# Performance work log

Measured on AMD Instinct MI355X. Metric: run time of the kernel, lower is better.

Reference implementation:

```python
import jax, jax.numpy as jnp
from jax import lax
import numpy as np

B, S, D, COMP = 4, 1024, 512, 4


def setup_inputs() -> dict:
    key = jax.random.key(0)
    x = jax.random.normal(key, (B * S, D), dtype=jnp.float32)
    return {"x": x, "comp_rate": COMP, "seqlen": S}


def _merge_step(x, t, seq):
    # x: [seq, D], compacted so the k = seq - t valid tokens occupy rows 0..k-1.
    xn = jnp.roll(x, -1, axis=0)  # x[i+1] (wrap value never selected among valid pairs)
    # dist only feeds argmax (non-differentiable), mirror torch exactly; stop_gradient
    # keeps the vjp from saving residuals for this dead-for-gradients path.
    xg = lax.stop_gradient(x)
    dist = jnp.sum(xg * jnp.roll(xg, -1, axis=0), axis=-1)  # scalar_product metric
    j = jnp.arange(x.shape[0])
    dist = jnp.where(j < seq - 1 - t, dist, -jnp.inf)  # k-1 valid adjacent pairs
    mid = jnp.argmax(dist)
    jm = j[:, None]
    # rows < mid keep, row mid becomes (x[mid]+x[mid+1])/2, rows > mid shift left by 1
    return jnp.where(jm < mid, x, jnp.where(jm == mid, (x + xn) * 0.5, xn))


def _merge_sample(x, steps, seq):
    def body(carry, t):
        return _merge_step(carry, t, seq), None
    x, _ = lax.scan(body, x, jnp.arange(steps))
    return x


def reference(x, comp_rate, seqlen):
    d = x.shape[-1]
    b = x.shape[0] // seqlen
    n_comp = seqlen // comp_rate
    steps = seqlen - n_comp
    xb = x.reshape(b, seqlen, d)
    merged = jax.vmap(lambda xs: _merge_sample(xs, steps, seqlen))(xb)
    # torch smart_merge concatenates per-sample results along dim 0
    return merged[:, :n_comp].reshape(b * n_comp, d)
```

## Files before the change

### kernel.cpp

```cpp
#include <hip/hip_runtime.h>
#include <math.h>

#define S 1024
#define D 512
#define NCOMP (S / 4)
#define STEPS (S - NCOMP)
#define NEG_INF (-__builtin_inff())

__device__ __forceinline__ int   f2i(float x) { return __builtin_bit_cast(int, x); }
__device__ __forceinline__ float i2f(int x)   { return __builtin_bit_cast(float, x); }
__device__ __forceinline__ int   rfl(int x)   { return __builtin_amdgcn_readfirstlane(x); }

__device__ __forceinline__ unsigned fkey(float f) {
    unsigned u = __builtin_bit_cast(unsigned, f);
    return (u & 0x80000000u) ? ~u : (u | 0x80000000u);
}
__device__ __forceinline__ float unfkey(unsigned k) {
    unsigned u = (k & 0x80000000u) ? (k & 0x7fffffffu) : ~k;
    return __builtin_bit_cast(float, u);
}

__device__ __forceinline__ float wave_sum63(float x) {
    x += i2f(__builtin_amdgcn_update_dpp(0, f2i(x), 0x111, 0xF, 0xF, true));
    x += i2f(__builtin_amdgcn_update_dpp(0, f2i(x), 0x112, 0xF, 0xF, true));
    x += i2f(__builtin_amdgcn_update_dpp(0, f2i(x), 0x114, 0xF, 0xF, true));
    x += i2f(__builtin_amdgcn_update_dpp(0, f2i(x), 0x118, 0xF, 0xF, true));
    x += i2f(__builtin_amdgcn_update_dpp(0, f2i(x), 0x142, 0xA, 0xF, true));
    x += i2f(__builtin_amdgcn_update_dpp(0, f2i(x), 0x143, 0xC, 0xF, true));
    return x;
}

#define AMAX_STEP(ctrl, rm) do {                                                        \
    unsigned ok_ = (unsigned)__builtin_amdgcn_update_dpp((int)key, (int)key, (ctrl), (rm), 0xF, false); \
    int      oi_ = __builtin_amdgcn_update_dpp(bi, bi, (ctrl), (rm), 0xF, false);        \
    bool tk_ = (ok_ > key) || ((ok_ == key) && (oi_ < bi));                              \
    key = tk_ ? ok_ : key; bi = tk_ ? oi_ : bi;                                          \
} while (0)

struct Row { float4 a, b; };

__device__ __forceinline__ Row row_load(const float* vals, int slot, int lane) {
    const float4* p = (const float4*)(vals + (size_t)slot * D);
    Row r; r.a = p[lane * 2]; r.b = p[lane * 2 + 1]; return r;
}
__device__ __forceinline__ void row_store(float* vals, int slot, int lane, Row r) {
    float4* p = (float4*)(vals + (size_t)slot * D);
    p[lane * 2] = r.a; p[lane * 2 + 1] = r.b;
}
__device__ __forceinline__ Row row_avg(Row x, Row y) {
    Row r;
    r.a.x = (x.a.x + y.a.x) * 0.5f; r.a.y = (x.a.y + y.a.y) * 0.5f;
    r.a.z = (x.a.z + y.a.z) * 0.5f; r.a.w = (x.a.w + y.a.w) * 0.5f;
    r.b.x = (x.b.x + y.b.x) * 0.5f; r.b.y = (x.b.y + y.b.y) * 0.5f;
    r.b.z = (x.b.z + y.b.z) * 0.5f; r.b.w = (x.b.w + y.b.w) * 0.5f;
    return r;
}
__device__ __forceinline__ float dot8_partial(Row x, Row y) {
    float acc = x.a.x * y.a.x;
    acc += x.a.y * y.a.y; acc += x.a.z * y.a.z; acc += x.a.w * y.a.w;
    acc += x.b.x * y.b.x; acc += x.b.y * y.b.y; acc += x.b.z * y.b.z; acc += x.b.w * y.b.w;
    return acc;
}
__device__ __forceinline__ int lsr(int s) { return ((unsigned)s < (unsigned)S) ? s : 0; }
__device__ __forceinline__ int lsl(int s) { return ((unsigned)s <= (unsigned)S) ? s : 0; }

__device__ __forceinline__ void lds_argmax(const float* dist, int lane, float& v1, int& i1) {
    float av[16];
#pragma unroll
    for (int k = 0; k < 16; ++k) av[k] = dist[lane + 64 * k];
    float v8[8]; int k8[8];
#pragma unroll
    for (int k = 0; k < 8; ++k) { bool tk = av[k+8] > av[k]; v8[k] = tk ? av[k+8] : av[k]; k8[k] = tk ? (k+8) : k; }
    float v4[4]; int k4[4];
#pragma unroll
    for (int k = 0; k < 4; ++k) { bool tk = v8[k+4] > v8[k]; v4[k] = tk ? v8[k+4] : v8[k]; k4[k] = tk ? k8[k+4] : k8[k]; }
    float v2[2]; int k2[2];
#pragma unroll
    for (int k = 0; k < 2; ++k) { bool tk = v4[k+2] > v4[k]; v2[k] = tk ? v4[k+2] : v4[k]; k2[k] = tk ? k4[k+2] : k4[k]; }
    bool tk1 = v2[1] > v2[0];
    float lv = tk1 ? v2[1] : v2[0];
    int   lk = tk1 ? k2[1] : k2[0];
    unsigned key = fkey(lv);
    int bi = lane | (lk << 6);
    AMAX_STEP(0x111, 0xF); AMAX_STEP(0x112, 0xF);
    AMAX_STEP(0x114, 0xF); AMAX_STEP(0x118, 0xF);
    AMAX_STEP(0x142, 0xA); AMAX_STEP(0x143, 0xC);
    i1 = __builtin_amdgcn_readlane(bi, 63);
    v1 = unfkey((unsigned)__builtin_amdgcn_readlane((int)key, 63));
}

__global__ __launch_bounds__(256) void init_kernel(const float* __restrict__ x,
                                                   float* __restrict__ vals,
                                                   float* __restrict__ out) {
    const int blk = blockIdx.x, b = blk >> 4, g = blk & 15;
    const int tid = threadIdx.x, lane = tid & 63, w = tid >> 6;
    const float* xb = x + (size_t)b * S * D;
    if (blk == 0 && tid == 0) *(int*)(out + 2048) = 0;
    if (vals != x) {
        float* vb = vals + (size_t)b * S * D;
        const float4* s4 = (const float4*)xb;
        float4* d4 = (float4*)vb;
        const int base = g * (S * D / 4 / 16);
        for (int i = tid; i < S * D / 4 / 16; i += 256) d4[base + i] = s4[base + i];
    }
    float* sd = out + (size_t)b * NCOMP * D;
#pragma unroll 1
    for (int j = 0; j < 16; ++j) {
        int pr = g * 64 + w * 16 + j;
        if (pr < S - 1) {
            Row A = row_load(xb, pr, lane);
            Row B = row_load(xb, pr + 1, lane);
            float t = wave_sum63(dot8_partial(A, B));
            if (lane == 63) sd[pr] = t;
        }
    }
    if (g == 0 && tid == 0) sd[S - 1] = NEG_INF;
}

__global__ __launch_bounds__(256, 1) void merge_kernel(float* __restrict__ vals,
                                                       float* __restrict__ out,
                                                       int nb) {
    const int blk = blockIdx.x, tid = threadIdx.x;
    int* flag = (int*)(out + 2048);

    if (blk >= nb) {
        float a0 = (float)tid * 0.5f + 1.0f, a1 = a0 + 0.25f, a2 = a0 + 0.5f, a3 = a0 + 0.75f;
        for (;;) {
#pragma unroll
            for (int i = 0; i < 16; ++i) {
                a0 = __builtin_fmaf(a0, 1.0000001f, 1.1920929e-7f);
                a1 = __builtin_fmaf(a1, 0.9999999f, 1.1920929e-7f);
                a2 = __builtin_fmaf(a2, 1.0000002f, 1.1920929e-7f);
                a3 = __builtin_fmaf(a3, 0.9999998f, 1.1920929e-7f);
            }
            if (__hip_atomic_load(flag, __ATOMIC_RELAXED, __HIP_MEMORY_SCOPE_AGENT) >= nb)
                break;
        }
        if (a0 + a1 + a2 + a3 == 1234.5678f) out[2049] = a0;
        return;
    }

    const int b = blk, lane = tid & 63, wave = tid >> 6;
    float* vb = vals + (size_t)b * S * D;
    float* aux = out + (size_t)b * NCOMP * D;
    const float* sd = aux;
    int* outIdx = (int*)(aux + S);

    if (wave != 0) {
        float acc = 0.0f;
        for (int s = wave - 1; s < S; s += 3) {
            Row rr = row_load(vb, s, lane);
            acc += rr.a.x + rr.b.w;
        }
        if (acc == 1234.5678f) out[2050] = acc;
        return;
    }

    __shared__ int4 links[S + 1];
    __shared__ float dist[S];

    for (int s = lane; s <= S; s += 64)
        links[s] = (s >= S) ? make_int4(S, S, S, 0)
                            : make_int4(s - 1, s + 1, (s + 2 <= S) ? (s + 2) : S, 0);
#pragma unroll
    for (int k = 0; k < 16; ++k) dist[lane + 64 * k] = sd[lane + 64 * k];

    float v1; int i1;
    lds_argmax(dist, lane, v1, i1);
    int m = i1;
    int4 L0 = links[m];
    int p = rfl(L0.x);
    int r = rfl(L0.y);
    int q = rfl(L0.z);
    bool hasp = (p >= 0), hasq = (q < S);
    int pp = hasp ? rfl(links[lsl(p)].x) : -1;
    int nq = hasq ? rfl(links[lsl(q)].y) : S;
    Row Rp  = row_load(vb, lsr(p),  lane);
    Row Rm  = row_load(vb, m,       lane);
    Row Rr  = row_load(vb, r,       lane);
    Row Rq  = row_load(vb, lsr(q),  lane);
    Row Rpp = row_load(vb, lsr(pp), lane);
    Row Rnq = row_load(vb, lsr(nq), lane);

#pragma unroll 1
    for (int t = 0; t < STEPS; ++t) {
        if (lane == 0) {
            links[m].y = q; links[m].z = nq;
            if (hasp) links[p].z = q;
            if (hasq) links[q].x = m;
            dist[m] = NEG_INF; dist[r] = NEG_INF;
            if (hasp) dist[p] = NEG_INF;
        }
        Row vm = row_avg(Rm, Rr);
        row_store(vb, m, lane, vm);
        if (t + 1 >= STEPS) break;

        float sp_ = wave_sum63(dot8_partial(Rp, vm));
        float sq_ = wave_sum63(dot8_partial(vm, Rq));
        float ndp = hasp ? i2f(__builtin_amdgcn_readlane(f2i(sp_), 63)) : NEG_INF;
        float ndm = hasq ? i2f(__builtin_amdgcn_readlane(f2i(sq_), 63)) : NEG_INF;

        lds_argmax(dist, lane, v1, i1);

        float best = v1; int bi = i1;
        if (hasp && (ndp > best || (ndp == best && p < bi))) { best = ndp; bi = p; }
        if (hasq && (ndm > best || (ndm == best && m < bi))) { best = ndm; bi = m; }
        const int m2 = bi;

        if (lane == 0) {
            if (hasp) dist[p] = ndp;
            if (hasq) dist[m] = ndm;
        }

        int4 Li = links[lsl(i1)];
        int p2 = rfl(Li.x);
        int r2 = rfl(Li.y);
        int q2 = rfl(Li.z);
        int4 Lp2 = links[lsl(p2)];
        int4 Lq2 = links[lsl(q2)];
        int pp2 = (p2 >= 0) ? rfl(Lp2.x) : -1;
        int nq2 = (q2 < S)  ? rfl(Lq2.y) : S;
        Row Sp  = (p2 == m)  ? vm : row_load(vb, lsr(p2),  lane);
        Row Si  = row_load(vb, lsr(i1), lane);
        Row Sr  = row_load(vb, lsr(r2), lane);
        Row Sq  = (q2 == m)  ? vm : row_load(vb, lsr(q2),  lane);
        Row Spp = (pp2 == m) ? vm : row_load(vb, lsr(pp2), lane);
        Row Snq = (nq2 == m) ? vm : row_load(vb, lsr(nq2), lane);

        if (m2 == m) {
            int nnq = S;
            if (nq < S) nnq = rfl(links[nq].y);
            Row Rnq2 = (nnq < S) ? row_load(vb, lsr(nnq), lane) : Rnq;
            Rm = vm; Rr = Rq; Rq = Rnq; Rnq = Rnq2;
            r = q; q = nq; nq = nnq;
            hasq = (q < S);
        } else if (m2 == p) {
            int npp = -1;
            if (pp >= 0) npp = rfl(links[pp].x);
            Row Rpp2 = (npp >= 0) ? row_load(vb, lsr(npp), lane) : Rpp;
            Rr = vm; Rm = Rp; Rp = Rpp; Rpp = Rpp2;
            r = m; m = p; p = pp; pp = npp;
            hasp = (p >= 0);
        } else {
            m = i1; p = p2; r = r2; q = q2; pp = pp2; nq = nq2;
            Rm = Si; Rr = Sr; Rp = Sp; Rq = Sq; Rpp = Spp; Rnq = Snq;
            hasp = (p >= 0); hasq = (q < S);
        }
    }

    if (lane == 0) {
        int s = 0;
        for (int i = 0; i < NCOMP; i += 2) {
            outIdx[i] = s;
            int4 Ls = links[s];
            if (i + 1 < NCOMP) outIdx[i + 1] = Ls.y;
            s = Ls.z;
        }
        __hip_atomic_fetch_add(flag, 1, __ATOMIC_RELAXED, __HIP_MEMORY_SCOPE_AGENT);
    }
}

__global__ __launch_bounds__(256) void gather_kernel(const float* __restrict__ vals,
                                                     float* __restrict__ out) {
    const int b = blockIdx.x, part = blockIdx.y;
    const float* vb = vals + (size_t)b * S * D;
    float* ob = out + (size_t)b * NCOMP * D;
    __shared__ int oi[NCOMP / 8];
    const int row0 = part * (NCOMP / 8);
    if (threadIdx.x < NCOMP / 8)
        oi[threadIdx.x] = ((const int*)(ob + S))[row0 + threadIdx.x];
    __syncthreads();
    const float4* v4 = (const float4*)vb;
    float4* o4 = (float4*)ob;
    const int per = (NCOMP / 8) * (D / 4);
    for (int idx = threadIdx.x; idx < per; idx += 256) {
        int row = idx >> 7, c = idx & 127;
        o4[(size_t)(row0 + row) * (D / 4) + c] = v4[(size_t)oi[row] * (D / 4) + c];
    }
}

extern "C" void kernel_launch(void* const* d_in, const int* in_sizes, int n_in,
                              void* d_out, int out_size, void* d_ws, size_t ws_size,
                              hipStream_t stream) {
    const float* x = (const float*)d_in[0];
    float* out = (float*)d_out;
    const int b = in_sizes[0] / (S * D);
    const size_t need = (size_t)in_sizes[0] * sizeof(float);
    float* vals = (ws_size >= need) ? (float*)d_ws : (float*)x;
    init_kernel<<<dim3(16 * b), dim3(256), 0, stream>>>(x, vals, out);
    merge_kernel<<<dim3(256), dim3(256), 0, stream>>>(vals, out, b);
    gather_kernel<<<dim3(b, 8), dim3(256), 0, stream>>>(vals, out);
}
```

Baseline: 1.031 ms.

## Hoist argmax and speculative row loads ahead of merge compute in serial loop

Stores a second-predecessor link in the .w field so the pp and nnq neighbors can be looked up with fewer dependent LDS reads. Moves the LDS argmax and all candidate row loads to the start of each step, before the averaged row is computed and stored, so their latency overlaps the dot products. Rows that may be stale because the previous step's global store has not yet landed are patched from a register copy (mprev/Rprev). This issues more loads per step and adds bookkeeping that must handle aliasing correctly.

```diff
diff --git a/kernel.cpp b/kernel.cpp
--- a/kernel.cpp
+++ b/kernel.cpp
@@ -161,9 +161,11 @@
 
     for (int s = lane; s <= S; s += 64)
         links[s] = (s >= S) ? make_int4(S, S, S, 0)
-                            : make_int4(s - 1, s + 1, (s + 2 <= S) ? (s + 2) : S, 0);
+                            : make_int4(s - 1, s + 1, (s + 2 <= S) ? (s + 2) : S, s - 2);
 #pragma unroll
     for (int k = 0; k < 16; ++k) dist[lane + 64 * k] = sd[lane + 64 * k];
+
+    const int* li32 = (const int*)links;
 
     float v1; int i1;
     lds_argmax(dist, lane, v1, i1);
@@ -181,16 +183,39 @@
     Row Rq  = row_load(vb, lsr(q),  lane);
     Row Rpp = row_load(vb, lsr(pp), lane);
     Row Rnq = row_load(vb, lsr(nq), lane);
+    int mprev = -1;
+    Row Rprev = Rm;
 
 #pragma unroll 1
     for (int t = 0; t < STEPS; ++t) {
         if (lane == 0) {
             links[m].y = q; links[m].z = nq;
             if (hasp) links[p].z = q;
-            if (hasq) links[q].x = m;
+            if (hasq) { links[q].x = m; links[q].w = p; links[lsl(nq)].w = m; }
             dist[m] = NEG_INF; dist[r] = NEG_INF;
             if (hasp) dist[p] = NEG_INF;
         }
+
+        int vnnq = li32[lsl(nq) * 4 + 1];
+        int vnpp = li32[lsl(pp) * 4 + 0];
+
+        lds_argmax(dist, lane, v1, i1);
+
+        int nnq = rfl(vnnq), npp = rfl(vnpp);
+        Row Rnqn = row_load(vb, lsr(nnq), lane);
+        Row Rppn = row_load(vb, lsr(npp), lane);
+
+        int4 Li = links[i1];
+        int p2 = rfl(Li.x), r2 = rfl(Li.y), q2 = rfl(Li.z), pp2 = rfl(Li.w);
+        int nq2 = rfl(li32[lsl(q2) * 4 + 1]);
+
+        Row Si  = row_load(vb, i1,       lane);
+        Row Sr  = row_load(vb, lsr(r2),  lane);
+        Row Sp  = row_load(vb, lsr(p2),  lane);
+        Row Sq  = row_load(vb, lsr(q2),  lane);
+        Row Spp = row_load(vb, lsr(pp2), lane);
+        Row Snq = row_load(vb, lsr(nq2), lane);
+
         Row vm = row_avg(Rm, Rr);
         row_store(vb, m, lane, vm);
         if (t + 1 >= STEPS) break;
@@ -200,8 +225,6 @@
         float ndp = hasp ? i2f(__builtin_amdgcn_readlane(f2i(sp_), 63)) : NEG_INF;
         float ndm = hasq ? i2f(__builtin_amdgcn_readlane(f2i(sq_), 63)) : NEG_INF;
 
-        lds_argmax(dist, lane, v1, i1);
-
         float best = v1; int bi = i1;
         if (hasp && (ndp > best || (ndp == best && p < bi))) { best = ndp; bi = p; }
         if (hasq && (ndm > best || (ndm == best && m < bi))) { best = ndm; bi = m; }
@@ -212,38 +235,36 @@
             if (hasq) dist[m] = ndm;
         }
 
-        int4 Li = links[lsl(i1)];
-        int p2 = rfl(Li.x);
-        int r2 = rfl(Li.y);
-        int q2 = rfl(Li.z);
-        int4 Lp2 = links[lsl(p2)];
-        int4 Lq2 = links[lsl(q2)];
-        int pp2 = (p2 >= 0) ? rfl(Lp2.x) : -1;
-        int nq2 = (q2 < S)  ? rfl(Lq2.y) : S;
-        Row Sp  = (p2 == m)  ? vm : row_load(vb, lsr(p2),  lane);
-        Row Si  = row_load(vb, lsr(i1), lane);
-        Row Sr  = row_load(vb, lsr(r2), lane);
-        Row Sq  = (q2 == m)  ? vm : row_load(vb, lsr(q2),  lane);
-        Row Spp = (pp2 == m) ? vm : row_load(vb, lsr(pp2), lane);
-        Row Snq = (nq2 == m) ? vm : row_load(vb, lsr(nq2), lane);
+        if (mprev >= 0) {
+            if (i1  == mprev) Si   = Rprev;
+            if (r2  == mprev) Sr   = Rprev;
+            if (p2  == mprev) Sp   = Rprev;
+            if (q2  == mprev) Sq   = Rprev;
+            if (pp2 == mprev) Spp  = Rprev;
+            if (nq2 == mprev) Snq  = Rprev;
+            if (nnq == mprev) Rnqn = Rprev;
+            if (npp == mprev) Rppn = Rprev;
+        }
 
         if (m2 == m) {
-            int nnq = S;
-            if (nq < S) nnq = rfl(links[nq].y);
-            Row Rnq2 = (nnq < S) ? row_load(vb, lsr(nnq), lane) : Rnq;
-            Rm = vm; Rr = Rq; Rq = Rnq; Rnq = Rnq2;
-            r = q; q = nq; nq = nnq;
-            hasq = (q < S);
+            Rm = vm; Rr = Rq; Rq = Rnq;
+            Rnq = (nnq < S) ? Rnqn : Rnq;
+            r = q; q = nq; nq = nnq; hasq = (q < S);
+            mprev = -1;
         } else if (m2 == p) {
-            int npp = -1;
-            if (pp >= 0) npp = rfl(links[pp].x);
-            Row Rpp2 = (npp >= 0) ? row_load(vb, lsr(npp), lane) : Rpp;
-            Rr = vm; Rm = Rp; Rp = Rpp; Rpp = Rpp2;
-            r = m; m = p; p = pp; pp = npp;
-            hasp = (p >= 0);
+            Rr = vm; Rm = Rp; Rp = Rpp;
+            Rpp = (npp >= 0) ? Rppn : Rpp;
+            r = m; m = p; p = pp; pp = npp; hasp = (p >= 0);
+            mprev = -1;
         } else {
+            const int mold = m;
+            mprev = mold; Rprev = vm;
+            Rm = Si; Rr = Sr;
+            Rp  = (p2  == mold) ? vm : Sp;
+            Rq  = (q2  == mold) ? vm : Sq;
+            Rpp = (pp2 == mold) ? vm : Spp;
+            Rnq = (nq2 == mold) ? vm : Snq;
             m = i1; p = p2; r = r2; q = q2; pp = pp2; nq = nq2;
-            Rm = Si; Rr = Sr; Rp = Sp; Rq = Sq; Rpp = Spp; Rnq = Snq;
             hasp = (p >= 0); hasq = (q < S);
         }
     }
```

Measured after the change: 1.281 ms. 1.24x slower.
